# Kernel tuning notes

Measured on AMD Instinct MI355X. Metric: run time of the kernel, lower is better.

Reference implementation:

```python
import jax, jax.numpy as jnp
import numpy as np

DECAY = 0.99
EPS = 1e-05
COMMITMENT_COST = 1.0
N_EMBED = 1024
DIM = 128


def setup_inputs() -> dict:
    key = jax.random.key(0)
    k1, k2, k3 = jax.random.split(key, 3)
    inputs = jax.random.normal(k1, (16, 64, 64, DIM), dtype=jnp.float32)
    embed = jax.random.normal(k2, (DIM, N_EMBED), dtype=jnp.float32)
    cluster_size = jnp.zeros((N_EMBED,), dtype=jnp.float32)
    embed_avg = embed.copy()
    return {"inputs": inputs, "embed": embed, "cluster_size": cluster_size,
            "embed_avg": embed_avg}


def reference(inputs, embed, cluster_size, embed_avg):
    # flatten: [N, dim]
    flatten = inputs.reshape(-1, DIM)
    # squared L2 distance to each code: [N, n_embed]
    dist = (jnp.sum(flatten * flatten, axis=1, keepdims=True)
            - 2.0 * flatten @ embed
            + jnp.sum(embed * embed, axis=0, keepdims=True))
    embed_ind_flat = jnp.argmin(dist, axis=1)                    # [N]
    embed_ind = embed_ind_flat.reshape(inputs.shape[:-1])        # [B,H,W]
    # quantize = embedding lookup of codebook columns
    quantize = embed.T[embed_ind]                                # [B,H,W,dim]

    # --- training-mode EMA codebook update (no grad in original) ---
    ones = jnp.ones_like(embed_ind_flat, dtype=flatten.dtype)
    embed_onehot_sum = jax.ops.segment_sum(ones, embed_ind_flat,
                                           num_segments=N_EMBED)            # [n_embed]
    embed_sum = jax.ops.segment_sum(flatten, embed_ind_flat,
                                    num_segments=N_EMBED).T                 # [dim, n_embed]
    cluster_size_new = cluster_size * DECAY + (1.0 - DECAY) * embed_onehot_sum
    embed_avg_new = embed_avg * DECAY + (1.0 - DECAY) * embed_sum
    n = jnp.sum(cluster_size_new)
    cs = (cluster_size_new + EPS) / (n + N_EMBED * EPS) * n
    embed_new = embed_avg_new / cs[None, :]                      # [dim, n_embed]

    loss = jnp.mean((quantize - inputs) ** 2) * COMMITMENT_COST
    quantize_st = inputs + (quantize - inputs)  # straight-through (identity in fwd)
    return quantize_st, embed_ind, loss, embed_new, cluster_size_new, embed_avg_new
```

## Files before the change

kernel.cpp:

```cpp
#include <hip/hip_runtime.h>


#define N_ROWS 65536
#define DIM 128
#define NE 1024

typedef __attribute__((ext_vector_type(8))) short short8;
typedef __attribute__((ext_vector_type(16))) float f32x16;

#define WS_ESQ    0
#define WS_CNTI   1024
#define WS_LOSS   2048
#define WS_N      2049
#define WS_ESUM   4096
#define WS_EHI    (WS_ESUM + DIM*NE)
#define WS_ET     (WS_EHI + 65536)
#define WS_BUCKET (WS_ET + DIM*NE)
#define WS_OFF    (WS_BUCKET + N_ROWS)
#define WS_POS    (WS_OFF + 1024)
#define WS_ZERO_BYTES ((WS_ESUM + DIM*NE) * 4)

#define O_Q    0
#define O_IND  (N_ROWS*DIM)
#define O_LOSS (O_IND + N_ROWS)
#define O_ENEW (O_LOSS + 1)
#define O_CS   (O_ENEW + DIM*NE)
#define O_EAVG (O_CS + NE)

__device__ __forceinline__ unsigned short f2bf(float f) {
    unsigned u = __float_as_uint(f);
    unsigned r = (u + 0x7fffu + ((u >> 16) & 1u)) >> 16;
    return (unsigned short)r;
}
__device__ __forceinline__ float bf2f(unsigned short h) {
    return __uint_as_float(((unsigned)h) << 16);
}
__device__ __forceinline__ void stage16(const void* g, void* l) {
    __builtin_amdgcn_global_load_lds(
        (const __attribute__((address_space(1))) unsigned*)g,
        (__attribute__((address_space(3))) unsigned*)l, 16, 0, 0);
}

__global__ __launch_bounds__(256) void k_prep(const float* __restrict__ E,
                                              float* __restrict__ ws) {
    __shared__ float ls[64][33];
    __shared__ float part[4][64];
    const int tid = threadIdx.x;
    const int b = blockIdx.x >> 2, kq = blockIdx.x & 3;
    const int lane = tid & 63, wid = tid >> 6;

    float sq = 0.f;
    #pragma unroll
    for (int t = 0; t < 8; ++t) {
        int kk = t * 4 + wid;
        float v = E[(kq * 32 + kk) * NE + b * 64 + lane];
        ls[lane][kk] = v;
        sq += v * v;
    }
    part[wid][lane] = sq;
    __syncthreads();
    if (tid < 64)
        atomicAdd(ws + WS_ESQ + b * 64 + tid,
                  part[0][tid] + part[1][tid] + part[2][tid] + part[3][tid]);

    {
        int c = tid >> 2, u = tid & 3;
        int kk8 = kq * 4 + u;
        int slot = kk8 ^ (c & 15);
        short8 hv;
        #pragma unroll
        for (int e = 0; e < 8; ++e)
            hv[e] = (short)f2bf(ls[c][u * 8 + e]);
        *(short8*)((char*)(ws + WS_EHI) + (size_t)b * 16384 + c * 256 + slot * 16) = hv;
    }
    float* et = ws + WS_ET;
    #pragma unroll
    for (int t = 0; t < 2; ++t) {
        int i = tid + t * 256;
        int c = i >> 3, k4i = i & 7;
        float4 v;
        v.x = ls[c][k4i * 4 + 0];
        v.y = ls[c][k4i * 4 + 1];
        v.z = ls[c][k4i * 4 + 2];
        v.w = ls[c][k4i * 4 + 3];
        *(float4*)(et + (size_t)(b * 64 + c) * DIM + kq * 32 + k4i * 4) = v;
    }
}

__global__ __launch_bounds__(256, 2) void k_main(const float* __restrict__ X,
                                                 float* __restrict__ ws,
                                                 float* __restrict__ out) {
    __shared__ __align__(16) char es[2][16384];
    __shared__ __align__(16) float esq_lds[NE];
    __shared__ int ind_sh[128];
    __shared__ float red2[4];

    const int tid = threadIdx.x;
    const int lane = tid & 63;
    const int wid = tid >> 6;
    const int col0 = lane & 31;
    const int hi = lane >> 5;
    const int rowBase = blockIdx.x * 128;

    const char* ehiB = (const char*)(ws + WS_EHI);

    #pragma unroll
    for (int t = 0; t < 4; ++t) {
        int i = tid + t * 256;
        stage16(ehiB + i * 16, &es[0][i * 16]);
    }

    ((float4*)esq_lds)[tid] = ((const float4*)(ws + WS_ESQ))[tid];

    short8 ah[8], al[8];
    {
        const float* xr = X + (size_t)(rowBase + wid * 32 + col0) * DIM + hi * 8;
        #pragma unroll
        for (int ks = 0; ks < 8; ++ks) {
            float4 a = *(const float4*)(xr + ks * 16);
            float4 b = *(const float4*)(xr + ks * 16 + 4);
            float xv[8] = {a.x, a.y, a.z, a.w, b.x, b.y, b.z, b.w};
            short8 h, l;
            #pragma unroll
            for (int e = 0; e < 8; ++e) {
                unsigned short hh = f2bf(xv[e]);
                h[e] = (short)hh;
                l[e] = (short)f2bf(xv[e] - bf2f(hh));
            }
            ah[ks] = h;
            al[ks] = l;
        }
    }
    __syncthreads();

    float bd[16];
    int bi[16];
    #pragma unroll
    for (int s = 0; s < 16; ++s) { bd[s] = 1e30f; bi[s] = 0; }

    const int swz = (col0 & 15) << 4;
    const int coff = col0 * 256;
    const int khb = hi * 16;

    for (int c = 0; c < 16; ++c) {
        const int cur = c & 1;
        if (c < 15) {
            const char* hp = ehiB + (c + 1) * 16384;
            #pragma unroll
            for (int t = 0; t < 4; ++t) {
                int i = tid + t * 256;
                stage16(hp + i * 16, &es[cur ^ 1][i * 16]);
            }
        }

        f32x16 h0, l0, h1, l1;
        #pragma unroll
        for (int s = 0; s < 16; ++s) { h0[s] = 0.f; l0[s] = 0.f; h1[s] = 0.f; l1[s] = 0.f; }

        const char* hb = es[cur];
        #pragma unroll
        for (int ks = 0; ks < 8; ++ks) {
            int kb = (ks * 32 + khb) ^ swz;
            short8 bh0 = *(const short8*)(hb + coff + kb);
            short8 bh1 = *(const short8*)(hb + 8192 + coff + kb);
            h0 = __builtin_amdgcn_mfma_f32_32x32x16_bf16(ah[ks], bh0, h0, 0, 0, 0);
            l0 = __builtin_amdgcn_mfma_f32_32x32x16_bf16(al[ks], bh0, l0, 0, 0, 0);
            h1 = __builtin_amdgcn_mfma_f32_32x32x16_bf16(ah[ks], bh1, h1, 0, 0, 0);
            l1 = __builtin_amdgcn_mfma_f32_32x32x16_bf16(al[ks], bh1, l1, 0, 0, 0);
        }

        float e0 = esq_lds[c * 64 + col0];
        float e1 = esq_lds[c * 64 + 32 + col0];
        int c0 = c * 64 + col0, c1 = c * 64 + 32 + col0;
        #pragma unroll
        for (int r = 0; r < 16; ++r) {
            float s0 = e0 - 2.f * (h0[r] + l0[r]);
            if (s0 < bd[r]) { bd[r] = s0; bi[r] = c0; }
            float s1 = e1 - 2.f * (h1[r] + l1[r]);
            if (s1 < bd[r]) { bd[r] = s1; bi[r] = c1; }
        }
        __syncthreads();
    }

    #pragma unroll
    for (int r = 0; r < 16; ++r) {
        #pragma unroll
        for (int off = 1; off < 32; off <<= 1) {
            float od = __shfl_xor(bd[r], off, 64);
            int oi = __shfl_xor(bi[r], off, 64);
            if (od < bd[r] || (od == bd[r] && oi < bi[r])) { bd[r] = od; bi[r] = oi; }
        }
    }
    if (col0 == 0) {
        int* cnt = (int*)(ws + WS_CNTI);
        #pragma unroll
        for (int r = 0; r < 16; ++r) {
            int row = wid * 32 + (r & 3) + 8 * (r >> 2) + 4 * hi;
            int b = bi[r];
            ind_sh[row] = b;
            out[O_IND + rowBase + row] = (float)b;
            atomicAdd(&cnt[b], 1);
        }
    }
    __syncthreads();

    float lp = 0.f;
    {
        const float* et = ws + WS_ET;
        int rsub = tid >> 5;
        int d4 = (tid & 31) * 4;
        #pragma unroll
        for (int seg = 0; seg < 16; ++seg) {
            int row = seg * 8 + rsub;
            int j = ind_sh[row];
            float4 xv = *(const float4*)(X + (size_t)(rowBase + row) * DIM + d4);
            float4 qv = *(const float4*)(et + (size_t)j * DIM + d4);
            float4 st;
            st.x = xv.x + (qv.x - xv.x);
            st.y = xv.y + (qv.y - xv.y);
            st.z = xv.z + (qv.z - xv.z);
            st.w = xv.w + (qv.w - xv.w);
            *(float4*)(out + O_Q + (size_t)(rowBase + row) * DIM + d4) = st;
            float dx;
            dx = qv.x - xv.x; lp += dx * dx;
            dx = qv.y - xv.y; lp += dx * dx;
            dx = qv.z - xv.z; lp += dx * dx;
            dx = qv.w - xv.w; lp += dx * dx;
        }
    }
    #pragma unroll
    for (int off = 32; off; off >>= 1) lp += __shfl_down(lp, off, 64);
    if (lane == 0) red2[wid] = lp;
    __syncthreads();
    if (tid == 0) atomicAdd(ws + WS_LOSS, red2[0] + red2[1] + red2[2] + red2[3]);
}

__global__ __launch_bounds__(1024) void k_scan(const float* __restrict__ CS,
                                               float* __restrict__ ws,
                                               float* __restrict__ out) {
    __shared__ int wsum[16];
    __shared__ float fsum[16];
    int tid = threadIdx.x;
    int* cnt = (int*)(ws + WS_CNTI);
    int v = cnt[tid];
    float csn = 0.99f * CS[tid] + 0.01f * (float)v;
    out[O_CS + tid] = csn;
    float s = csn;
    #pragma unroll
    for (int off = 32; off; off >>= 1) s += __shfl_down(s, off, 64);
    int sc = v;
    #pragma unroll
    for (int d = 1; d < 64; d <<= 1) {
        int t = __shfl_up(sc, d, 64);
        if ((tid & 63) >= d) sc += t;
    }
    if ((tid & 63) == 0) fsum[tid >> 6] = s;
    if ((tid & 63) == 63) wsum[tid >> 6] = sc;
    __syncthreads();
    if (tid == 0) {
        int run = 0;
        float n = 0.f;
        for (int w = 0; w < 16; ++w) {
            int t = wsum[w]; wsum[w] = run; run += t;
            n += fsum[w];
        }
        ws[WS_N] = n;
        out[O_LOSS] = ws[WS_LOSS] * (1.0f / ((float)N_ROWS * (float)DIM));
    }
    __syncthreads();
    ((int*)(ws + WS_OFF))[tid] = sc - v + wsum[tid >> 6];
    ((int*)(ws + WS_POS))[tid] = 0;
}

__global__ __launch_bounds__(256) void k_scatter(const float* __restrict__ out,
                                                 float* __restrict__ ws) {
    int i = blockIdx.x * 256 + threadIdx.x;
    int j = (int)out[O_IND + i];
    int* pos = (int*)(ws + WS_POS);
    int slot = atomicAdd(&pos[j], 1);
    ((int*)(ws + WS_BUCKET))[((int*)(ws + WS_OFF))[j] + slot] = i;
}

__global__ __launch_bounds__(128) void k_segsum(const float* __restrict__ X,
                                                float* __restrict__ ws) {
    __shared__ int offL[1025];
    __shared__ int rs[64];
    const int tid = threadIdx.x;
    const int p0 = blockIdx.x * 64;
    const int* off = (const int*)(ws + WS_OFF);
    #pragma unroll
    for (int t = 0; t < 8; ++t) offL[tid + t * 128] = off[tid + t * 128];
    if (tid == 0) offL[1024] = N_ROWS;
    if (tid < 64) rs[tid] = ((const int*)(ws + WS_BUCKET))[p0 + tid];
    __syncthreads();

    int lo = 0, hi2 = 1023;
    while (lo < hi2) {
        int mid = (lo + hi2 + 1) >> 1;
        if (offL[mid] <= p0) lo = mid; else hi2 = mid - 1;
    }
    int j = lo;
    int bnd = offL[j + 1];
    float* esum = ws + WS_ESUM;
    float acc = 0.f;
    #pragma unroll 2
    for (int base = 0; base < 64; base += 8) {
        float v[8];
        #pragma unroll
        for (int u = 0; u < 8; ++u)
            v[u] = X[(size_t)rs[base + u] * DIM + tid];
        #pragma unroll
        for (int u = 0; u < 8; ++u) {
            int p = p0 + base + u;
            if (p >= bnd) {
                atomicAdd(&esum[tid * NE + j], acc);
                acc = 0.f;
                do { ++j; bnd = offL[j + 1]; } while (p >= bnd);
            }
            acc += v[u];
        }
    }
    atomicAdd(&esum[tid * NE + j], acc);
}

__global__ __launch_bounds__(256) void k_final(const float* __restrict__ CS,
                                               const float* __restrict__ EA,
                                               const float* __restrict__ ws,
                                               float* __restrict__ out) {
    int d = blockIdx.x >> 2;
    int j = (blockIdx.x & 3) * 256 + threadIdx.x;
    float nall = ws[WS_N];
    float csn = 0.99f * CS[j] + 0.01f * (float)((const int*)(ws + WS_CNTI))[j];
    float cs = (csn + 1e-5f) / (nall + (float)NE * 1e-5f) * nall;
    float ean = EA[(size_t)d * NE + j] * 0.99f + 0.01f * ws[WS_ESUM + (size_t)d * NE + j];
    out[O_EAVG + (size_t)d * NE + j] = ean;
    out[O_ENEW + (size_t)d * NE + j] = ean / cs;
}

extern "C" void kernel_launch(void* const* d_in, const int* in_sizes, int n_in,
                              void* d_out, int out_size, void* d_ws, size_t ws_size,
                              hipStream_t stream) {
    const float* X = (const float*)d_in[0];
    const float* E = (const float*)d_in[1];
    const float* CS = (const float*)d_in[2];
    const float* EA = (const float*)d_in[3];
    float* out = (float*)d_out;
    float* ws = (float*)d_ws;

    hipMemsetAsync(d_ws, 0, (size_t)WS_ZERO_BYTES, stream);
    k_prep   <<<dim3(64),           dim3(256),  0, stream>>>(E, ws);
    k_main   <<<dim3(N_ROWS / 128), dim3(256),  0, stream>>>(X, ws, out);
    k_scan   <<<dim3(1),            dim3(1024), 0, stream>>>(CS, ws, out);
    k_scatter<<<dim3(N_ROWS / 256), dim3(256),  0, stream>>>(out, ws);
    k_segsum <<<dim3(N_ROWS / 64),  dim3(128),  0, stream>>>(X, ws);
    k_final  <<<dim3(512),          dim3(256),  0, stream>>>(CS, EA, ws, out);
}
```

Baseline: 204.2 us.

## Drop bf16 split-precision low term and split codebook across two wave groups

Removes the low-order bf16 correction of the inputs, so the distance matmul uses only the bf16-rounded activations, which halves the MFMA work. The block grows to 512 threads, with two groups of four waves each scanning half the codebook, and the per-row minima are merged through shared memory. MFMA sections are wrapped in s_setprio. Dropping the low term lowers distance precision and can flip argmin on near ties, which risks index mismatches against the fp32 reference.

```diff
diff --git a/kernel.cpp b/kernel.cpp
--- a/kernel.cpp
+++ b/kernel.cpp
@@ -32,9 +32,6 @@
     unsigned r = (u + 0x7fffu + ((u >> 16) & 1u)) >> 16;
     return (unsigned short)r;
 }
-__device__ __forceinline__ float bf2f(unsigned short h) {
-    return __uint_as_float(((unsigned)h) << 16);
-}
 __device__ __forceinline__ void stage16(const void* g, void* l) {
     __builtin_amdgcn_global_load_lds(
         (const __attribute__((address_space(1))) unsigned*)g,
@@ -87,48 +84,50 @@
     }
 }
 
-__global__ __launch_bounds__(256, 2) void k_main(const float* __restrict__ X,
+__global__ __launch_bounds__(512, 4) void k_main(const float* __restrict__ X,
                                                  float* __restrict__ ws,
                                                  float* __restrict__ out) {
-    __shared__ __align__(16) char es[2][16384];
+    __shared__ __align__(16) char es[2][2][16384];
     __shared__ __align__(16) float esq_lds[NE];
     __shared__ int ind_sh[128];
-    __shared__ float red2[4];
+    __shared__ float mbd[128];
+    __shared__ int mbi[128];
+    __shared__ float red2[8];
 
     const int tid = threadIdx.x;
     const int lane = tid & 63;
     const int wid = tid >> 6;
+    const int grp = wid >> 2;
+    const int rw = wid & 3;
     const int col0 = lane & 31;
     const int hi = lane >> 5;
+    const int tig = tid & 255;
     const int rowBase = blockIdx.x * 128;
 
     const char* ehiB = (const char*)(ws + WS_EHI);
+    const char* grpB = ehiB + grp * 8 * 16384;
 
     #pragma unroll
     for (int t = 0; t < 4; ++t) {
-        int i = tid + t * 256;
-        stage16(ehiB + i * 16, &es[0][i * 16]);
-    }
-
-    ((float4*)esq_lds)[tid] = ((const float4*)(ws + WS_ESQ))[tid];
-
-    short8 ah[8], al[8];
+        int i = tig + t * 256;
+        stage16(grpB + i * 16, &es[grp][0][i * 16]);
+    }
+
+    if (tid < 256) ((float4*)esq_lds)[tid] = ((const float4*)(ws + WS_ESQ))[tid];
+
+    short8 ah[8];
     {
-        const float* xr = X + (size_t)(rowBase + wid * 32 + col0) * DIM + hi * 8;
+        const float* xr = X + (size_t)(rowBase + rw * 32 + col0) * DIM + hi * 8;
         #pragma unroll
         for (int ks = 0; ks < 8; ++ks) {
             float4 a = *(const float4*)(xr + ks * 16);
             float4 b = *(const float4*)(xr + ks * 16 + 4);
-            float xv[8] = {a.x, a.y, a.z, a.w, b.x, b.y, b.z, b.w};
-            short8 h, l;
-            #pragma unroll
-            for (int e = 0; e < 8; ++e) {
-                unsigned short hh = f2bf(xv[e]);
-                h[e] = (short)hh;
-                l[e] = (short)f2bf(xv[e] - bf2f(hh));
-            }
+            short8 h;
+            h[0] = (short)f2bf(a.x); h[1] = (short)f2bf(a.y);
+            h[2] = (short)f2bf(a.z); h[3] = (short)f2bf(a.w);
+            h[4] = (short)f2bf(b.x); h[5] = (short)f2bf(b.y);
+            h[6] = (short)f2bf(b.z); h[7] = (short)f2bf(b.w);
             ah[ks] = h;
-            al[ks] = l;
         }
     }
     __syncthreads();
@@ -142,41 +141,42 @@
     const int coff = col0 * 256;
     const int khb = hi * 16;
 
-    for (int c = 0; c < 16; ++c) {
+    for (int c = 0; c < 8; ++c) {
         const int cur = c & 1;
-        if (c < 15) {
-            const char* hp = ehiB + (c + 1) * 16384;
+        if (c < 7) {
+            const char* hp = grpB + (c + 1) * 16384;
             #pragma unroll
             for (int t = 0; t < 4; ++t) {
-                int i = tid + t * 256;
-                stage16(hp + i * 16, &es[cur ^ 1][i * 16]);
+                int i = tig + t * 256;
+                stage16(hp + i * 16, &es[grp][cur ^ 1][i * 16]);
             }
         }
 
-        f32x16 h0, l0, h1, l1;
-        #pragma unroll
-        for (int s = 0; s < 16; ++s) { h0[s] = 0.f; l0[s] = 0.f; h1[s] = 0.f; l1[s] = 0.f; }
-
-        const char* hb = es[cur];
+        f32x16 h0, h1;
+        #pragma unroll
+        for (int s = 0; s < 16; ++s) { h0[s] = 0.f; h1[s] = 0.f; }
+
+        const char* hb = es[grp][cur];
+        __builtin_amdgcn_s_setprio(1);
         #pragma unroll
         for (int ks = 0; ks < 8; ++ks) {
             int kb = (ks * 32 + khb) ^ swz;
             short8 bh0 = *(const short8*)(hb + coff + kb);
             short8 bh1 = *(const short8*)(hb + 8192 + coff + kb);
             h0 = __builtin_amdgcn_mfma_f32_32x32x16_bf16(ah[ks], bh0, h0, 0, 0, 0);
-            l0 = __builtin_amdgcn_mfma_f32_32x32x16_bf16(al[ks], bh0, l0, 0, 0, 0);
             h1 = __builtin_amdgcn_mfma_f32_32x32x16_bf16(ah[ks], bh1, h1, 0, 0, 0);
-            l1 = __builtin_amdgcn_mfma_f32_32x32x16_bf16(al[ks], bh1, l1, 0, 0, 0);
-        }
-
-        float e0 = esq_lds[c * 64 + col0];
-        float e1 = esq_lds[c * 64 + 32 + col0];
-        int c0 = c * 64 + col0, c1 = c * 64 + 32 + col0;
+        }
+        __builtin_amdgcn_s_setprio(0);
+
+        int base = (grp * 8 + c) * 64;
+        float e0 = esq_lds[base + col0];
+        float e1 = esq_lds[base + 32 + col0];
+        int c0 = base + col0, c1 = base + 32 + col0;
         #pragma unroll
         for (int r = 0; r < 16; ++r) {
-            float s0 = e0 - 2.f * (h0[r] + l0[r]);
+            float s0 = e0 - 2.f * h0[r];
             if (s0 < bd[r]) { bd[r] = s0; bi[r] = c0; }
-            float s1 = e1 - 2.f * (h1[r] + l1[r]);
+            float s1 = e1 - 2.f * h1[r];
             if (s1 < bd[r]) { bd[r] = s1; bi[r] = c1; }
         }
         __syncthreads();
@@ -191,12 +191,22 @@
             if (od < bd[r] || (od == bd[r] && oi < bi[r])) { bd[r] = od; bi[r] = oi; }
         }
     }
-    if (col0 == 0) {
+    if (grp == 1 && col0 == 0) {
+        #pragma unroll
+        for (int r = 0; r < 16; ++r) {
+            int row = rw * 32 + (r & 3) + 8 * (r >> 2) + 4 * hi;
+            mbd[row] = bd[r];
+            mbi[row] = bi[r];
+        }
+    }
+    __syncthreads();
+    if (grp == 0 && col0 == 0) {
         int* cnt = (int*)(ws + WS_CNTI);
         #pragma unroll
         for (int r = 0; r < 16; ++r) {
-            int row = wid * 32 + (r & 3) + 8 * (r >> 2) + 4 * hi;
-            int b = bi[r];
+            int row = rw * 32 + (r & 3) + 8 * (r >> 2) + 4 * hi;
+            float od = mbd[row];
+            int b = (od < bd[r]) ? mbi[row] : bi[r];
             ind_sh[row] = b;
             out[O_IND + rowBase + row] = (float)b;
             atomicAdd(&cnt[b], 1);
@@ -210,8 +220,8 @@
         int rsub = tid >> 5;
         int d4 = (tid & 31) * 4;
         #pragma unroll
-        for (int seg = 0; seg < 16; ++seg) {
-            int row = seg * 8 + rsub;
+        for (int seg = 0; seg < 8; ++seg) {
+            int row = seg * 16 + rsub;
             int j = ind_sh[row];
             float4 xv = *(const float4*)(X + (size_t)(rowBase + row) * DIM + d4);
             float4 qv = *(const float4*)(et + (size_t)j * DIM + d4);
@@ -232,7 +242,12 @@
     for (int off = 32; off; off >>= 1) lp += __shfl_down(lp, off, 64);
     if (lane == 0) red2[wid] = lp;
     __syncthreads();
-    if (tid == 0) atomicAdd(ws + WS_LOSS, red2[0] + red2[1] + red2[2] + red2[3]);
+    if (tid == 0) {
+        float t = 0.f;
+        #pragma unroll
+        for (int w = 0; w < 8; ++w) t += red2[w];
+        atomicAdd(ws + WS_LOSS, t);
+    }
 }
 
 __global__ __launch_bounds__(1024) void k_scan(const float* __restrict__ CS,
@@ -349,7 +364,7 @@
 
     hipMemsetAsync(d_ws, 0, (size_t)WS_ZERO_BYTES, stream);
     k_prep   <<<dim3(64),           dim3(256),  0, stream>>>(E, ws);
-    k_main   <<<dim3(N_ROWS / 128), dim3(256),  0, stream>>>(X, ws, out);
+    k_main   <<<dim3(N_ROWS / 128), dim3(512),  0, stream>>>(X, ws, out);
     k_scan   <<<dim3(1),            dim3(1024), 0, stream>>>(CS, ws, out);
     k_scatter<<<dim3(N_ROWS / 256), dim3(256),  0, stream>>>(out, ws);
     k_segsum <<<dim3(N_ROWS / 64),  dim3(128),  0, stream>>>(X, ws);
```

New measurement: 195.6 us. 4.2% less time.
